# Kernel optimization log

Hardware: AMD Instinct MI355X
Metric: run time of the kernel (lower is better)

The kernel has to match this reference:

```python
import jax, jax.numpy as jnp
import numpy as np

B, N, D_IN, D, E, HEADS = 64, 512, 33, 32, 8192, 4
L, K_HOP, FF = 2, 2, 64  # num_layers, k_hop, dim_feedforward=2*d_out


def setup_inputs():
    key = jax.random.key(0)
    ks = iter(jax.random.split(key, 40))
    def nrm(shape, s=0.05):
        return jax.random.normal(next(ks), shape, jnp.float32) * s
    return {
        "H": jax.random.normal(next(ks), (B, N, D_IN), jnp.float32),
        "edge_index": jax.random.randint(next(ks), (2, E), 0, N, jnp.int32),
        # ObsEmbedding: Linear(33,32) ReLU Linear(32,32) ReLU LayerNorm(32)
        "emb_W1": nrm((D_IN, 32)), "emb_b1": jnp.zeros((32,), jnp.float32),
        "emb_W2": nrm((32, 32)), "emb_b2": jnp.zeros((32,), jnp.float32),
        "emb_ln_g": jnp.ones((32,), jnp.float32), "emb_ln_b": jnp.zeros((32,), jnp.float32),
        # per transformer layer: k_hop PNA-style GNN structure extractor
        # each hop: concat(self, mean, max, sum) -> Linear(4D, D), ReLU
        "gnn_W": nrm((L, K_HOP, 4 * D, D)), "gnn_b": jnp.zeros((L, K_HOP, D), jnp.float32),
        # structure-aware attention: Q,K from GNN-extracted features, V from x
        "Wq": nrm((L, D, D)), "Wk": nrm((L, D, D)), "Wv": nrm((L, D, D)), "Wo": nrm((L, D, D)),
        "bn1_g": jnp.ones((L, D), jnp.float32), "bn1_b": jnp.zeros((L, D), jnp.float32),
        "ff_W1": nrm((L, D, FF)), "ff_b1": jnp.zeros((L, FF), jnp.float32),
        "ff_W2": nrm((L, FF, D)), "ff_b2": jnp.zeros((L, D), jnp.float32),
        "bn2_g": jnp.ones((L, D), jnp.float32), "bn2_b": jnp.zeros((L, D), jnp.float32),
        # final node-level head Linear(d_model, num_class=d_out)
        "out_W": nrm((D, D)), "out_b": jnp.zeros((D,), jnp.float32),
    }


def _ln(x, g, b):
    m = x.mean(-1, keepdims=True)
    v = x.var(-1, keepdims=True)
    return (x - m) * jax.lax.rsqrt(v + 1e-5) * g + b


def _bn(x, g, b):  # batch_norm over all nodes of all graphs (training-mode stats)
    m = x.mean((0, 1))
    v = x.var((0, 1))
    return (x - m) * jax.lax.rsqrt(v + 1e-5) * g + b


def reference(H, edge_index, emb_W1, emb_b1, emb_W2, emb_b2, emb_ln_g, emb_ln_b,
              gnn_W, gnn_b, Wq, Wk, Wv, Wo, bn1_g, bn1_b,
              ff_W1, ff_b1, ff_W2, ff_b2, bn2_g, bn2_b, out_W, out_b):
    src, dst = edge_index[0], edge_index[1]
    # ObsEmbedding
    x = jax.nn.relu(H @ emb_W1 + emb_b1)
    x = jax.nn.relu(x @ emb_W2 + emb_b2)
    x = _ln(x, emb_ln_g, emb_ln_b)  # [B,N,D]
    cnt = jnp.zeros((N, 1), x.dtype).at[dst].add(1.0)  # in-degree, shared across batch
    dh = D // HEADS
    inv_sqrt_dh = np.float32(1.0 / np.sqrt(dh))
    for l in range(L):
        # --- k-hop structure extractor (PNA-style multi-aggregator message passing) ---
        h = x
        for k in range(K_HOP):
            msg = h[:, src]                                   # [B,E,D] gather
            s = jnp.zeros_like(h).at[:, dst].add(msg)         # sum aggregate
            mean = s / jnp.maximum(cnt, 1.0)
            mx = jnp.full_like(h, -1e30).at[:, dst].max(msg)  # max aggregate
            mx = jnp.where(cnt > 0, mx, 0.0)
            h = jax.nn.relu(jnp.concatenate([h, mean, mx, s], -1) @ gnn_W[l, k] + gnn_b[l, k])
        # --- structure-aware multi-head attention (full attention within graph) ---
        q = (h @ Wq[l]).reshape(B, N, HEADS, dh)
        kk = (h @ Wk[l]).reshape(B, N, HEADS, dh)
        v = (x @ Wv[l]).reshape(B, N, HEADS, dh)
        att = jax.nn.softmax(jnp.einsum("bqhd,bkhd->bhqk", q, kk) * inv_sqrt_dh, axis=-1)
        o = jnp.einsum("bhqk,bkhd->bqhd", att, v).reshape(B, N, D) @ Wo[l]
        x = _bn(x + o, bn1_g[l], bn1_b[l])
        f = jax.nn.relu(x @ ff_W1[l] + ff_b1[l]) @ ff_W2[l] + ff_b2[l]
        x = _bn(x + f, bn2_g[l], bn2_b[l])
    return x @ out_W + out_b  # [B,N,d_out], eval mode so dropout is identity
```

## Files before the change

### kernel.cpp

```cpp
#include <hip/hip_runtime.h>
#include <hip/hip_bf16.h>

#define BB 64
#define NN 512
#define DIN 33
#define DD 32
#define EE 8192
#define NHEADS 4
#define DH 8
#define FFD 64

typedef __attribute__((ext_vector_type(4))) float f32x4;
typedef __attribute__((ext_vector_type(4))) short bf16x4;

static __device__ __forceinline__ short f2bf(float x) {
    unsigned u = __float_as_uint(x);
    u = (u + 0x7FFFu + ((u >> 16) & 1u)) >> 16;
    return (short)u;
}

static __device__ __forceinline__ unsigned pack_trunc(float a, float b) {
    return (__float_as_uint(a) >> 16) | (__float_as_uint(b) & 0xFFFF0000u);
}

static __device__ __forceinline__ void mfma16(f32x4& d, bf16x4 a, bf16x4 b) {
#if __has_builtin(__builtin_amdgcn_mfma_f32_16x16x16bf16_1k)
    d = __builtin_amdgcn_mfma_f32_16x16x16bf16_1k(a, b, d, 0, 0, 0);
#else
    asm volatile("s_nop 1\n\tv_mfma_f32_16x16x16_bf16 %0, %1, %2, %0\n\ts_nop 7"
                 : "+v"(d) : "v"(a), "v"(b));
#endif
}

__global__ __launch_bounds__(512) void k_csr(const int* __restrict__ ei,
                                             float* __restrict__ cnt_f,
                                             int* __restrict__ csr_off,
                                             int* __restrict__ csr_src,
                                             float* __restrict__ stats) {
    __shared__ int cnt_s[NN];
    __shared__ int off_s[NN + 1];
    int tid = threadIdx.x;
    cnt_s[tid] = 0;
    if (tid < 256) stats[tid] = 0.f;
    __syncthreads();
    const int* src = ei;
    const int* dst = ei + EE;
    for (int e = tid; e < EE; e += 512) atomicAdd(&cnt_s[dst[e]], 1);
    __syncthreads();
    if (tid == 0) {
        int acc = 0;
        for (int n = 0; n < NN; ++n) { off_s[n] = acc; acc += cnt_s[n]; }
        off_s[NN] = acc;
    }
    __syncthreads();
    cnt_f[tid] = (float)cnt_s[tid];
    csr_off[tid] = off_s[tid];
    if (tid == 0) csr_off[NN] = off_s[NN];
    cnt_s[tid] = off_s[tid];
    __syncthreads();
    for (int e = tid; e < EE; e += 512) {
        int d = dst[e];
        int p = atomicAdd(&cnt_s[d], 1);
        csr_src[p] = src[e];
    }
}

__global__ __launch_bounds__(256) void k_emb(const float* __restrict__ H,
                                             const float* __restrict__ W1, const float* __restrict__ b1,
                                             const float* __restrict__ W2, const float* __restrict__ b2,
                                             const float* __restrict__ g,  const float* __restrict__ be,
                                             float* __restrict__ xb, float* __restrict__ xt) {
    __shared__ float sW1[DIN * DD];
    __shared__ float sW2[DD * DD];
    __shared__ float sb1[DD], sb2[DD], sg[DD], sbe[DD];
    __shared__ float sin_[8][DIN + 3];
    int tid = threadIdx.x;
    for (int i = tid; i < DIN * DD; i += 256) sW1[i] = W1[i];
    for (int i = tid; i < DD * DD; i += 256) sW2[i] = W2[i];
    if (tid < DD) { sb1[tid] = b1[tid]; sb2[tid] = b2[tid]; sg[tid] = g[tid]; sbe[tid] = be[tid]; }
    int grp = tid >> 5, lane = tid & 31;
    size_t node = (size_t)blockIdx.x * 8 + grp;
    const float* hrow = H + node * DIN;
    sin_[grp][lane] = hrow[lane];
    if (lane == 0) sin_[grp][32] = hrow[32];
    __syncthreads();
    float acc = sb1[lane];
    #pragma unroll
    for (int i = 0; i < DIN; ++i) acc += sin_[grp][i] * sW1[i * DD + lane];
    acc = fmaxf(acc, 0.f);
    float acc2 = sb2[lane];
    #pragma unroll
    for (int i = 0; i < DD; ++i) acc2 += __shfl(acc, i, 32) * sW2[i * DD + lane];
    acc2 = fmaxf(acc2, 0.f);
    float s = acc2;
    for (int off = 16; off; off >>= 1) s += __shfl_xor(s, off, 32);
    float m = s * (1.f / 32.f);
    float dv = acc2 - m;
    float sq = dv * dv;
    for (int off = 16; off; off >>= 1) sq += __shfl_xor(sq, off, 32);
    float var = sq * (1.f / 32.f);
    float v = dv * rsqrtf(var + 1e-5f) * sg[lane] + sbe[lane];
    xb[node * DD + lane] = v;
    int b = (int)(node >> 9), n = (int)(node & 511);
    xt[(size_t)n * 2048 + b * DD + lane] = v;
}

__global__ __launch_bounds__(256) void k_gnn(const float* __restrict__ gsrc, float* __restrict__ ht,
                                             const float* __restrict__ cnt_f,
                                             const int* __restrict__ csr_off,
                                             const int* __restrict__ csr_src,
                                             const float* __restrict__ W, const float* __restrict__ bias,
                                             int do_qkv,
                                             const float* __restrict__ xv_src,
                                             const float* __restrict__ Wq, const float* __restrict__ Wk,
                                             const float* __restrict__ Wv,
                                             short* __restrict__ qb2, short* __restrict__ kb2,
                                             short* __restrict__ vb2) {
    __shared__ short conc[32 * 132];
    __shared__ short sWt[32 * 132];
    __shared__ short sWqT[32 * 36], sWkT[32 * 36], sWvT[32 * 36];
    __shared__ short h_lds[32 * 36], x_lds[32 * 36];
    __shared__ float sb[DD];
    int tid = threadIdx.x;
    int n = blockIdx.x >> 1, half = blockIdx.x & 1;
    for (int i = tid; i < 128 * DD; i += 256) {
        int k = i >> 5, d = i & 31;
        sWt[d * 132 + k] = f2bf(W[i]);
    }
    if (tid < DD) sb[tid] = bias[tid];
    if (do_qkv) {
        const float isq = 0.35355339059327373f;
        for (int i = tid; i < 1024; i += 256) {
            int k = i >> 5, col = i & 31;
            sWqT[col * 36 + k] = f2bf(Wq[i] * isq);
            sWkT[col * 36 + k] = f2bf(Wk[i]);
            sWvT[col * 36 + k] = f2bf(Wv[i]);
        }
        int bl = tid >> 3, d0 = (tid & 7) * 4;
        float4 x4 = *(const float4*)&xv_src[(size_t)n * 2048 + half * 1024 + bl * 32 + d0];
        bf16x4 xp; xp.x = f2bf(x4.x); xp.y = f2bf(x4.y); xp.z = f2bf(x4.z); xp.w = f2bf(x4.w);
        *(bf16x4*)&x_lds[bl * 36 + d0] = xp;
    }
    const float* xbase = gsrc + (size_t)half * 1024 + tid * 4;
    float4 hv = *(const float4*)&xbase[(size_t)n * 2048];
    float4 s = {0.f, 0.f, 0.f, 0.f};
    float4 mx = {-1e30f, -1e30f, -1e30f, -1e30f};
    int beg = csr_off[n], end = csr_off[n + 1];
    int idx = beg;
    for (; idx + 3 < end; idx += 4) {
        int s0 = csr_src[idx], s1 = csr_src[idx + 1], s2 = csr_src[idx + 2], s3 = csr_src[idx + 3];
        float4 v0 = *(const float4*)&xbase[(size_t)s0 * 2048];
        float4 v1 = *(const float4*)&xbase[(size_t)s1 * 2048];
        float4 v2 = *(const float4*)&xbase[(size_t)s2 * 2048];
        float4 v3 = *(const float4*)&xbase[(size_t)s3 * 2048];
        s.x += (v0.x + v1.x) + (v2.x + v3.x);
        s.y += (v0.y + v1.y) + (v2.y + v3.y);
        s.z += (v0.z + v1.z) + (v2.z + v3.z);
        s.w += (v0.w + v1.w) + (v2.w + v3.w);
        mx.x = fmaxf(fmaxf(mx.x, v0.x), fmaxf(v1.x, fmaxf(v2.x, v3.x)));
        mx.y = fmaxf(fmaxf(mx.y, v0.y), fmaxf(v1.y, fmaxf(v2.y, v3.y)));
        mx.z = fmaxf(fmaxf(mx.z, v0.z), fmaxf(v1.z, fmaxf(v2.z, v3.z)));
        mx.w = fmaxf(fmaxf(mx.w, v0.w), fmaxf(v1.w, fmaxf(v2.w, v3.w)));
    }
    for (; idx < end; ++idx) {
        int s0 = csr_src[idx];
        float4 v0 = *(const float4*)&xbase[(size_t)s0 * 2048];
        s.x += v0.x; s.y += v0.y; s.z += v0.z; s.w += v0.w;
        mx.x = fmaxf(mx.x, v0.x); mx.y = fmaxf(mx.y, v0.y);
        mx.z = fmaxf(mx.z, v0.z); mx.w = fmaxf(mx.w, v0.w);
    }
    float c = cnt_f[n];
    float rinv = 1.f / fmaxf(c, 1.f);
    if (!(c > 0.f)) { mx.x = 0.f; mx.y = 0.f; mx.z = 0.f; mx.w = 0.f; }
    int bl = tid >> 3, d0 = (tid & 7) * 4;
    short* cp = &conc[bl * 132];
    bf16x4 t;
    t.x = f2bf(hv.x); t.y = f2bf(hv.y); t.z = f2bf(hv.z); t.w = f2bf(hv.w);
    *(bf16x4*)&cp[d0] = t;
    t.x = f2bf(s.x * rinv); t.y = f2bf(s.y * rinv); t.z = f2bf(s.z * rinv); t.w = f2bf(s.w * rinv);
    *(bf16x4*)&cp[32 + d0] = t;
    t.x = f2bf(mx.x); t.y = f2bf(mx.y); t.z = f2bf(mx.z); t.w = f2bf(mx.w);
    *(bf16x4*)&cp[64 + d0] = t;
    t.x = f2bf(s.x); t.y = f2bf(s.y); t.z = f2bf(s.z); t.w = f2bf(s.w);
    *(bf16x4*)&cp[96 + d0] = t;
    __syncthreads();
    int wid = tid >> 6, lane = tid & 63;
    int cc = lane & 15, g = lane >> 4;
    int arow = (wid >> 1) * 16 + cc;
    int bcol = (wid & 1) * 16 + cc;
    f32x4 acc = {0.f, 0.f, 0.f, 0.f};
    #pragma unroll
    for (int ks = 0; ks < 8; ++ks) {
        bf16x4 af = *(const bf16x4*)&conc[arow * 132 + ks * 16 + g * 4];
        bf16x4 bfr = *(const bf16x4*)&sWt[bcol * 132 + ks * 16 + g * 4];
        mfma16(acc, af, bfr);
    }
    float bia = sb[bcol];
    int brow = (wid >> 1) * 16 + g * 4;
    if (!do_qkv) {
        float* obase = &ht[(size_t)n * 2048 + half * 1024 + bcol];
        #pragma unroll
        for (int r = 0; r < 4; ++r) {
            obase[(size_t)(brow + r) * DD] = fmaxf(acc[r] + bia, 0.f);
        }
        return;
    }
    #pragma unroll
    for (int r = 0; r < 4; ++r) {
        h_lds[(brow + r) * 36 + bcol] = f2bf(fmaxf(acc[r] + bia, 0.f));
    }
    __syncthreads();
    int tr = wid >> 1, tc = wid & 1;
    f32x4 qa = {0.f, 0.f, 0.f, 0.f}, ka = qa, va = qa;
    #pragma unroll
    for (int ks = 0; ks < 2; ++ks) {
        bf16x4 ha = *(const bf16x4*)&h_lds[(tr * 16 + cc) * 36 + ks * 16 + g * 4];
        bf16x4 xa = *(const bf16x4*)&x_lds[(tr * 16 + cc) * 36 + ks * 16 + g * 4];
        bf16x4 wq = *(const bf16x4*)&sWqT[(tc * 16 + cc) * 36 + ks * 16 + g * 4];
        bf16x4 wk = *(const bf16x4*)&sWkT[(tc * 16 + cc) * 36 + ks * 16 + g * 4];
        bf16x4 wv = *(const bf16x4*)&sWvT[(tc * 16 + cc) * 36 + ks * 16 + g * 4];
        mfma16(qa, ha, wq);
        mfma16(ka, ha, wk);
        mfma16(va, xa, wv);
    }
    int dcol = tc * 16 + cc;
    size_t base = ((size_t)(half * 32 + tr * 16 + g * 4) * NN + n) * DD + dcol;
    #pragma unroll
    for (int r = 0; r < 4; ++r) {
        size_t p = base + (size_t)r * (NN * DD);
        qb2[p] = f2bf(qa[r]);
        kb2[p] = f2bf(ka[r]);
        vb2[p] = f2bf(va[r]);
    }
}

__global__ __launch_bounds__(256) void k_attn_proj(const short* __restrict__ qb2,
                                                   const short* __restrict__ kb2,
                                                   const short* __restrict__ vb2,
                                                   const float* __restrict__ x,
                                                   const float* __restrict__ Wo,
                                                   float* __restrict__ t,
                                                   float* __restrict__ stats) {
    __shared__ short Vt[NHEADS * DH * 528];
    __shared__ short Ot[64 * 36];
    __shared__ short sWoT[DD * 36];
    __shared__ float rs[4][DD], rq[4][DD];
    int bid = blockIdx.x;
    int qs = bid & 7, b = bid >> 3;
    int tid = threadIdx.x;

    for (int i = tid; i < 1024; i += 256) {
        int k = i >> 5, col = i & 31;
        sWoT[col * 36 + k] = f2bf(Wo[i]);
    }
    {
        size_t g0 = ((size_t)b * NN + tid * 2) * DD;
        #pragma unroll
        for (int h2 = 0; h2 < 4; ++h2) {
            uint4 v0 = *(const uint4*)&vb2[g0 + h2 * 8];
            uint4 v1 = *(const uint4*)&vb2[g0 + DD + h2 * 8];
            unsigned* vt = (unsigned*)&Vt[h2 * DH * 528];
            vt[0 * 264 + tid] = (v0.x & 0xFFFFu) | (v1.x << 16);
            vt[1 * 264 + tid] = (v0.x >> 16)     | (v1.x & 0xFFFF0000u);
            vt[2 * 264 + tid] = (v0.y & 0xFFFFu) | (v1.y << 16);
            vt[3 * 264 + tid] = (v0.y >> 16)     | (v1.y & 0xFFFF0000u);
            vt[4 * 264 + tid] = (v0.z & 0xFFFFu) | (v1.z << 16);
            vt[5 * 264 + tid] = (v0.z >> 16)     | (v1.z & 0xFFFF0000u);
            vt[6 * 264 + tid] = (v0.w & 0xFFFFu) | (v1.w << 16);
            vt[7 * 264 + tid] = (v0.w >> 16)     | (v1.w & 0xFFFF0000u);
        }
    }
    __syncthreads();

    int h = tid >> 6, lane = tid & 63;
    int c = lane & 15, g = lane >> 4;
    int c7 = c & 7;
    bf16x4 z4 = {0, 0, 0, 0};
    bf16x4 qf0 = z4, qf1 = z4, qf2 = z4, qf3 = z4;
    if (g < 2) {
        const short* qbase = &qb2[(((size_t)b * NN + qs * 64) * DD) + h * DH + g * 4];
        qf0 = *(const bf16x4*)&qbase[(size_t)(c) * DD];
        qf1 = *(const bf16x4*)&qbase[(size_t)(16 + c) * DD];
        qf2 = *(const bf16x4*)&qbase[(size_t)(32 + c) * DD];
        qf3 = *(const bf16x4*)&qbase[(size_t)(48 + c) * DD];
    }
    const short* kbase = &kb2[((size_t)b * NN) * DD + h * DH + g * 4];
    float l0 = 0.f, l1 = 0.f, l2 = 0.f, l3 = 0.f;
    f32x4 o0 = {0.f, 0.f, 0.f, 0.f}, o1 = o0, o2 = o0, o3 = o0;
    union U { unsigned u[2]; bf16x4 v4; };

    for (int kc = 0; kc < 32; ++kc) {
        bf16x4 kf = z4;
        if (g < 2) kf = *(const bf16x4*)&kbase[(size_t)(kc * 16 + c) * DD];
        bf16x4 vf = z4;
        {
            bf16x4 vl = *(const bf16x4*)&Vt[(h * DH + c7) * 528 + kc * 16 + g * 4];
            if (c < 8) vf = vl;
        }
        f32x4 st0 = {0.f, 0.f, 0.f, 0.f}, st1 = st0, st2 = st0, st3 = st0;
        mfma16(st0, kf, qf0);
        mfma16(st1, kf, qf1);
        mfma16(st2, kf, qf2);
        mfma16(st3, kf, qf3);
        {
            float p0 = __expf(st0[0]), p1 = __expf(st0[1]), p2 = __expf(st0[2]), p3 = __expf(st0[3]);
            l0 += (p0 + p1) + (p2 + p3);
            U pu; pu.u[0] = pack_trunc(p0, p1); pu.u[1] = pack_trunc(p2, p3);
            mfma16(o0, vf, pu.v4);
        }
        {
            float p0 = __expf(st1[0]), p1 = __expf(st1[1]), p2 = __expf(st1[2]), p3 = __expf(st1[3]);
            l1 += (p0 + p1) + (p2 + p3);
            U pu; pu.u[0] = pack_trunc(p0, p1); pu.u[1] = pack_trunc(p2, p3);
            mfma16(o1, vf, pu.v4);
        }
        {
            float p0 = __expf(st2[0]), p1 = __expf(st2[1]), p2 = __expf(st2[2]), p3 = __expf(st2[3]);
            l2 += (p0 + p1) + (p2 + p3);
            U pu; pu.u[0] = pack_trunc(p0, p1); pu.u[1] = pack_trunc(p2, p3);
            mfma16(o2, vf, pu.v4);
        }
        {
            float p0 = __expf(st3[0]), p1 = __expf(st3[1]), p2 = __expf(st3[2]), p3 = __expf(st3[3]);
            l3 += (p0 + p1) + (p2 + p3);
            U pu; pu.u[0] = pack_trunc(p0, p1); pu.u[1] = pack_trunc(p2, p3);
            mfma16(o3, vf, pu.v4);
        }
    }
    l0 += __shfl_xor(l0, 16, 64); l0 += __shfl_xor(l0, 32, 64);
    l1 += __shfl_xor(l1, 16, 64); l1 += __shfl_xor(l1, 32, 64);
    l2 += __shfl_xor(l2, 16, 64); l2 += __shfl_xor(l2, 32, 64);
    l3 += __shfl_xor(l3, 16, 64); l3 += __shfl_xor(l3, 32, 64);
    if (g < 2) {
        float inv0 = 1.f / l0, inv1 = 1.f / l1, inv2 = 1.f / l2, inv3 = 1.f / l3;
        int fb = h * DH + g * 4;
        #pragma unroll
        for (int r = 0; r < 4; ++r) {
            Ot[(c) * 36 + fb + r]      = f2bf(o0[r] * inv0);
            Ot[(16 + c) * 36 + fb + r] = f2bf(o1[r] * inv1);
            Ot[(32 + c) * 36 + fb + r] = f2bf(o2[r] * inv2);
            Ot[(48 + c) * 36 + fb + r] = f2bf(o3[r] * inv3);
        }
    }
    __syncthreads();
    f32x4 pa0 = {0.f, 0.f, 0.f, 0.f}, pa1 = pa0;
    #pragma unroll
    for (int ks = 0; ks < 2; ++ks) {
        bf16x4 af = *(const bf16x4*)&Ot[(h * 16 + c) * 36 + ks * 16 + g * 4];
        bf16x4 b0 = *(const bf16x4*)&sWoT[c * 36 + ks * 16 + g * 4];
        bf16x4 b1 = *(const bf16x4*)&sWoT[(16 + c) * 36 + ks * 16 + g * 4];
        mfma16(pa0, af, b0);
        mfma16(pa1, af, b1);
    }
    float ls0 = 0.f, lq0 = 0.f, ls1 = 0.f, lq1 = 0.f;
    size_t rowbase = ((size_t)b * NN + qs * 64 + h * 16 + g * 4) * DD;
    #pragma unroll
    for (int r = 0; r < 4; ++r) {
        float xv0 = x[rowbase + (size_t)r * DD + c];
        float tv0 = xv0 + pa0[r];
        t[rowbase + (size_t)r * DD + c] = tv0;
        ls0 += tv0; lq0 += tv0 * tv0;
        float xv1 = x[rowbase + (size_t)r * DD + 16 + c];
        float tv1 = xv1 + pa1[r];
        t[rowbase + (size_t)r * DD + 16 + c] = tv1;
        ls1 += tv1; lq1 += tv1 * tv1;
    }
    ls0 += __shfl_xor(ls0, 16, 64); ls0 += __shfl_xor(ls0, 32, 64);
    lq0 += __shfl_xor(lq0, 16, 64); lq0 += __shfl_xor(lq0, 32, 64);
    ls1 += __shfl_xor(ls1, 16, 64); ls1 += __shfl_xor(ls1, 32, 64);
    lq1 += __shfl_xor(lq1, 16, 64); lq1 += __shfl_xor(lq1, 32, 64);
    if (g == 0) {
        rs[h][c] = ls0; rs[h][16 + c] = ls1;
        rq[h][c] = lq0; rq[h][16 + c] = lq1;
    }
    __syncthreads();
    if (tid < DD) {
        float a = (rs[0][tid] + rs[1][tid]) + (rs[2][tid] + rs[3][tid]);
        float b2 = (rq[0][tid] + rq[1][tid]) + (rq[2][tid] + rq[3][tid]);
        atomicAdd(&stats[tid], a);
        atomicAdd(&stats[DD + tid], b2);
    }
}

__global__ __launch_bounds__(256) void k_ff(const float* __restrict__ t, const float* __restrict__ stats,
                                            const float* __restrict__ g1, const float* __restrict__ be1,
                                            const float* __restrict__ W1, const float* __restrict__ fb1,
                                            const float* __restrict__ W2, const float* __restrict__ fb2,
                                            float* __restrict__ t2, float* __restrict__ stats2) {
    __shared__ short x1b[64 * 36];
    __shared__ float x1f[64 * 33];
    __shared__ short hm[64 * 68];
    __shared__ short sW1T[FFD * 36];
    __shared__ short sW2T[DD * 68];
    __shared__ float sc[DD], sm[DD], sbe[DD], sb2v[DD];
    __shared__ float sb1v[FFD];
    __shared__ float rs[4][DD], rq[4][DD];
    int tid = threadIdx.x;
    for (int i = tid; i < 2048; i += 256) {
        int k = i >> 6, col = i & 63;
        sW1T[col * 36 + k] = f2bf(W1[i]);
        int k2 = i >> 5, col2 = i & 31;
        sW2T[col2 * 68 + k2] = f2bf(W2[i]);
    }
    if (tid < DD) {
        float mean = stats[tid] * (1.f / 32768.f);
        float var  = stats[DD + tid] * (1.f / 32768.f) - mean * mean;
        sc[tid] = rsqrtf(var + 1e-5f) * g1[tid];
        sm[tid] = mean; sbe[tid] = be1[tid]; sb2v[tid] = fb2[tid];
    }
    if (tid < FFD) sb1v[tid] = fb1[tid];
    __syncthreads();
    size_t node0 = (size_t)blockIdx.x * 64;
    {
        int row = tid >> 2, cb = (tid & 3) * 8;
        const float* tp = &t[(node0 + row) * DD + cb];
        float4 a = *(const float4*)tp;
        float4 bq = *(const float4*)(tp + 4);
        float v0 = (a.x - sm[cb + 0]) * sc[cb + 0] + sbe[cb + 0];
        float v1 = (a.y - sm[cb + 1]) * sc[cb + 1] + sbe[cb + 1];
        float v2 = (a.z - sm[cb + 2]) * sc[cb + 2] + sbe[cb + 2];
        float v3 = (a.w - sm[cb + 3]) * sc[cb + 3] + sbe[cb + 3];
        float v4 = (bq.x - sm[cb + 4]) * sc[cb + 4] + sbe[cb + 4];
        float v5 = (bq.y - sm[cb + 5]) * sc[cb + 5] + sbe[cb + 5];
        float v6 = (bq.z - sm[cb + 6]) * sc[cb + 6] + sbe[cb + 6];
        float v7 = (bq.w - sm[cb + 7]) * sc[cb + 7] + sbe[cb + 7];
        float* xf = &x1f[row * 33 + cb];
        xf[0] = v0; xf[1] = v1; xf[2] = v2; xf[3] = v3;
        xf[4] = v4; xf[5] = v5; xf[6] = v6; xf[7] = v7;
        bf16x4 p0; p0.x = f2bf(v0); p0.y = f2bf(v1); p0.z = f2bf(v2); p0.w = f2bf(v3);
        bf16x4 p1; p1.x = f2bf(v4); p1.y = f2bf(v5); p1.z = f2bf(v6); p1.w = f2bf(v7);
        *(bf16x4*)&x1b[row * 36 + cb] = p0;
        *(bf16x4*)&x1b[row * 36 + cb + 4] = p1;
    }
    __syncthreads();
    int w = tid >> 6, lane = tid & 63, c = lane & 15, g = lane >> 4;
    f32x4 m0 = {0.f, 0.f, 0.f, 0.f}, m1 = m0, m2 = m0, m3 = m0;
    #pragma unroll
    for (int ks = 0; ks < 2; ++ks) {
        bf16x4 af = *(const bf16x4*)&x1b[(w * 16 + c) * 36 + ks * 16 + g * 4];
        mfma16(m0, af, *(const bf16x4*)&sW1T[(c) * 36 + ks * 16 + g * 4]);
        mfma16(m1, af, *(const bf16x4*)&sW1T[(16 + c) * 36 + ks * 16 + g * 4]);
        mfma16(m2, af, *(const bf16x4*)&sW1T[(32 + c) * 36 + ks * 16 + g * 4]);
        mfma16(m3, af, *(const bf16x4*)&sW1T[(48 + c) * 36 + ks * 16 + g * 4]);
    }
    {
        float b0 = sb1v[c], b1 = sb1v[16 + c], b2 = sb1v[32 + c], b3 = sb1v[48 + c];
        #pragma unroll
        for (int r = 0; r < 4; ++r) {
            short* hr = &hm[(w * 16 + g * 4 + r) * 68];
            hr[c]      = f2bf(fmaxf(m0[r] + b0, 0.f));
            hr[16 + c] = f2bf(fmaxf(m1[r] + b1, 0.f));
            hr[32 + c] = f2bf(fmaxf(m2[r] + b2, 0.f));
            hr[48 + c] = f2bf(fmaxf(m3[r] + b3, 0.f));
        }
    }
    __syncthreads();
    f32x4 f0 = {0.f, 0.f, 0.f, 0.f}, f1 = f0;
    #pragma unroll
    for (int ks = 0; ks < 4; ++ks) {
        bf16x4 af = *(const bf16x4*)&hm[(w * 16 + c) * 68 + ks * 16 + g * 4];
        mfma16(f0, af, *(const bf16x4*)&sW2T[(c) * 68 + ks * 16 + g * 4]);
        mfma16(f1, af, *(const bf16x4*)&sW2T[(16 + c) * 68 + ks * 16 + g * 4]);
    }
    float ls0 = 0.f, lq0 = 0.f, ls1 = 0.f, lq1 = 0.f;
    float bb0 = sb2v[c], bb1 = sb2v[16 + c];
    #pragma unroll
    for (int r = 0; r < 4; ++r) {
        int row = w * 16 + g * 4 + r;
        float tv0 = x1f[row * 33 + c] + f0[r] + bb0;
        t2[(node0 + row) * DD + c] = tv0;
        ls0 += tv0; lq0 += tv0 * tv0;
        float tv1 = x1f[row * 33 + 16 + c] + f1[r] + bb1;
        t2[(node0 + row) * DD + 16 + c] = tv1;
        ls1 += tv1; lq1 += tv1 * tv1;
    }
    ls0 += __shfl_xor(ls0, 16, 64); ls0 += __shfl_xor(ls0, 32, 64);
    lq0 += __shfl_xor(lq0, 16, 64); lq0 += __shfl_xor(lq0, 32, 64);
    ls1 += __shfl_xor(ls1, 16, 64); ls1 += __shfl_xor(ls1, 32, 64);
    lq1 += __shfl_xor(lq1, 16, 64); lq1 += __shfl_xor(lq1, 32, 64);
    if (g == 0) {
        rs[w][c] = ls0; rs[w][16 + c] = ls1;
        rq[w][c] = lq0; rq[w][16 + c] = lq1;
    }
    __syncthreads();
    if (tid < DD) {
        float a = (rs[0][tid] + rs[1][tid]) + (rs[2][tid] + rs[3][tid]);
        float bsum = (rq[0][tid] + rq[1][tid]) + (rq[2][tid] + rq[3][tid]);
        atomicAdd(&stats2[tid], a);
        atomicAdd(&stats2[DD + tid], bsum);
    }
}

__global__ __launch_bounds__(256) void k_bn2(const float* __restrict__ t2, const float* __restrict__ stats2,
                                             const float* __restrict__ g, const float* __restrict__ be,
                                             float* __restrict__ xout, float* __restrict__ xtout,
                                             const float* __restrict__ outW, const float* __restrict__ outb,
                                             float* __restrict__ fout, int do_proj) {
    __shared__ float sW[DD * DD];
    int tid = threadIdx.x;
    if (do_proj) for (int i = tid; i < DD * DD; i += 256) sW[i] = outW[i];
    __syncthreads();
    int grp = tid >> 5, lane = tid & 31;
    float mean  = stats2[lane] * (1.f / 32768.f);
    float var   = stats2[DD + lane] * (1.f / 32768.f) - mean * mean;
    float scale = rsqrtf(var + 1e-5f) * g[lane];
    float shift = be[lane];
    size_t node = (size_t)blockIdx.x * 8 + grp;
    float tv = t2[node * DD + lane];
    float xv = (tv - mean) * scale + shift;
    xout[node * DD + lane] = xv;
    int b = (int)(node >> 9), n = (int)(node & 511);
    xtout[(size_t)n * 2048 + b * DD + lane] = xv;
    if (do_proj) {
        float acc = outb[lane];
        #pragma unroll
        for (int i = 0; i < DD; ++i) acc += __shfl(xv, i, 32) * sW[i * DD + lane];
        fout[node * DD + lane] = acc;
    }
}

extern "C" void kernel_launch(void* const* d_in, const int* in_sizes, int n_in,
                              void* d_out, int out_size, void* d_ws, size_t ws_size,
                              hipStream_t stream) {
    const float* H    = (const float*)d_in[0];
    const int*   ei   = (const int*)  d_in[1];
    const float* eW1  = (const float*)d_in[2];
    const float* eb1  = (const float*)d_in[3];
    const float* eW2  = (const float*)d_in[4];
    const float* eb2  = (const float*)d_in[5];
    const float* elg  = (const float*)d_in[6];
    const float* elb  = (const float*)d_in[7];
    const float* gW   = (const float*)d_in[8];
    const float* gb   = (const float*)d_in[9];
    const float* Wq   = (const float*)d_in[10];
    const float* Wk   = (const float*)d_in[11];
    const float* Wv   = (const float*)d_in[12];
    const float* Wo   = (const float*)d_in[13];
    const float* bn1g = (const float*)d_in[14];
    const float* bn1b = (const float*)d_in[15];
    const float* fW1  = (const float*)d_in[16];
    const float* fb1  = (const float*)d_in[17];
    const float* fW2  = (const float*)d_in[18];
    const float* fb2  = (const float*)d_in[19];
    const float* bn2g = (const float*)d_in[20];
    const float* bn2b = (const float*)d_in[21];
    const float* oW   = (const float*)d_in[22];
    const float* obv  = (const float*)d_in[23];
    float* out = (float*)d_out;

    float* ws = (float*)d_ws;
    const size_t BIGSZ = (size_t)BB * NN * DD;
    float* xb = ws;
    float* xt = ws + 1 * BIGSZ;
    float* hA = ws + 2 * BIGSZ;
    float* hB = ws + 3 * BIGSZ;
    short* qb2 = (short*)(ws + 4 * BIGSZ);
    short* kb2 = qb2 + BIGSZ;
    short* vb2 = (short*)(ws + 5 * BIGSZ);
    float* tb = ws + 7 * BIGSZ;
    float* smalls = ws + 8 * BIGSZ;
    float* cnt_f   = smalls;
    int*   csr_off = (int*)(smalls + 512);
    int*   csr_src = (int*)(smalls + 512 + 516);
    float* stats   = smalls + 512 + 516 + 8192;

    k_csr<<<1, 512, 0, stream>>>(ei, cnt_f, csr_off, csr_src, stats);
    k_emb<<<BB * NN / 8, 256, 0, stream>>>(H, eW1, eb1, eW2, eb2, elg, elb, xb, xt);

    for (int l = 0; l < 2; ++l) {
        const float* gW0 = gW + (size_t)(l * 2 + 0) * 128 * DD;
        const float* gW1 = gW + (size_t)(l * 2 + 1) * 128 * DD;
        const float* gb0 = gb + (size_t)(l * 2 + 0) * DD;
        const float* gb1 = gb + (size_t)(l * 2 + 1) * DD;
        float* st1 = stats + l * 128;
        float* st2 = stats + l * 128 + 64;
        k_gnn<<<NN * 2, 256, 0, stream>>>(xt, hA, cnt_f, csr_off, csr_src, gW0, gb0,
                                          0, nullptr, nullptr, nullptr, nullptr,
                                          nullptr, nullptr, nullptr);
        k_gnn<<<NN * 2, 256, 0, stream>>>(hA, nullptr, cnt_f, csr_off, csr_src, gW1, gb1,
                                          1, xt, Wq + l * DD * DD, Wk + l * DD * DD,
                                          Wv + l * DD * DD, qb2, kb2, vb2);
        k_attn_proj<<<BB * 8, 256, 0, stream>>>(qb2, kb2, vb2, xb, Wo + l * DD * DD, tb, st1);
        k_ff<<<512, 256, 0, stream>>>(tb, st1, bn1g + l * DD, bn1b + l * DD,
                                      fW1 + l * DD * FFD, fb1 + l * FFD,
                                      fW2 + l * FFD * DD, fb2 + l * DD,
                                      hB, st2);
        k_bn2<<<BB * NN / 8, 256, 0, stream>>>(hB, st2, bn2g + l * DD, bn2b + l * DD,
                                               xb, xt, oW, obv, out, (l == 1) ? 1 : 0);
    }
}
```

Baseline: 218.9 us.

## Fold BN2 normalization into downstream kernels and drop separate bn2 pass

```diff
diff --git a/kernel.cpp b/kernel.cpp
--- a/kernel.cpp
+++ b/kernel.cpp
@@ -38,7 +38,7 @@
                                              int* __restrict__ csr_src,
                                              float* __restrict__ stats) {
     __shared__ int cnt_s[NN];
-    __shared__ int off_s[NN + 1];
+    __shared__ int wsum[8];
     int tid = threadIdx.x;
     cnt_s[tid] = 0;
     if (tid < 256) stats[tid] = 0.f;
@@ -47,16 +47,28 @@
     const int* dst = ei + EE;
     for (int e = tid; e < EE; e += 512) atomicAdd(&cnt_s[dst[e]], 1);
     __syncthreads();
+    int c = cnt_s[tid];
+    int lane = tid & 63, w = tid >> 6;
+    int sc_ = c;
+    #pragma unroll
+    for (int off = 1; off < 64; off <<= 1) {
+        int nv = __shfl_up(sc_, off, 64);
+        if (lane >= off) sc_ += nv;
+    }
+    if (lane == 63) wsum[w] = sc_;
+    __syncthreads();
     if (tid == 0) {
-        int acc = 0;
-        for (int n = 0; n < NN; ++n) { off_s[n] = acc; acc += cnt_s[n]; }
-        off_s[NN] = acc;
-    }
-    __syncthreads();
-    cnt_f[tid] = (float)cnt_s[tid];
-    csr_off[tid] = off_s[tid];
-    if (tid == 0) csr_off[NN] = off_s[NN];
-    cnt_s[tid] = off_s[tid];
+        int a = 0;
+        #pragma unroll
+        for (int i = 0; i < 8; ++i) { int t = wsum[i]; wsum[i] = a; a += t; }
+    }
+    __syncthreads();
+    int excl = sc_ - c + wsum[w];
+    cnt_f[tid] = (float)c;
+    csr_off[tid] = excl;
+    if (tid == 511) csr_off[NN] = excl + c;
+    __syncthreads();
+    cnt_s[tid] = excl;
     __syncthreads();
     for (int e = tid; e < EE; e += 512) {
         int d = dst[e];
@@ -105,30 +117,137 @@
     xt[(size_t)n * 2048 + b * DD + lane] = v;
 }
 
-__global__ __launch_bounds__(256) void k_gnn(const float* __restrict__ gsrc, float* __restrict__ ht,
-                                             const float* __restrict__ cnt_f,
-                                             const int* __restrict__ csr_off,
-                                             const int* __restrict__ csr_src,
-                                             const float* __restrict__ W, const float* __restrict__ bias,
-                                             int do_qkv,
-                                             const float* __restrict__ xv_src,
-                                             const float* __restrict__ Wq, const float* __restrict__ Wk,
-                                             const float* __restrict__ Wv,
-                                             short* __restrict__ qb2, short* __restrict__ kb2,
-                                             short* __restrict__ vb2) {
+__global__ __launch_bounds__(256) void k_gnn1(const float* __restrict__ src, float* __restrict__ ht,
+                                              const float* __restrict__ cnt_f,
+                                              const int* __restrict__ csr_off,
+                                              const int* __restrict__ csr_src,
+                                              const float* __restrict__ W, const float* __restrict__ bias,
+                                              const float* __restrict__ bnstats,
+                                              const float* __restrict__ bng, const float* __restrict__ bnb) {
+    __shared__ short conc[32 * 132];
+    __shared__ short sWt[32 * 132];
+    __shared__ float sb[DD];
+    __shared__ float scv[DD], offv[DD];
+    int tid = threadIdx.x;
+    int n = blockIdx.x >> 1, half = blockIdx.x & 1;
+    for (int i = tid; i < 128 * DD; i += 256) {
+        int k = i >> 5, d = i & 31;
+        sWt[d * 132 + k] = f2bf(W[i]);
+    }
+    if (tid < DD) {
+        sb[tid] = bias[tid];
+        if (bnstats) {
+            float mean = bnstats[tid] * (1.f / 32768.f);
+            float var  = bnstats[DD + tid] * (1.f / 32768.f) - mean * mean;
+            float sc = rsqrtf(var + 1e-5f) * bng[tid];
+            scv[tid] = sc; offv[tid] = bnb[tid] - mean * sc;
+        } else { scv[tid] = 1.f; offv[tid] = 0.f; }
+    }
+    __syncthreads();
+    float4 sc4, of4;
+    { int d0 = (tid * 4) & 31;
+      sc4.x = scv[d0]; sc4.y = scv[d0 + 1]; sc4.z = scv[d0 + 2]; sc4.w = scv[d0 + 3];
+      of4.x = offv[d0]; of4.y = offv[d0 + 1]; of4.z = offv[d0 + 2]; of4.w = offv[d0 + 3]; }
+    const float* xbase = src + (size_t)half * 1024 + tid * 4;
+    float4 hv = *(const float4*)&xbase[(size_t)n * 2048];
+    hv.x = fmaf(hv.x, sc4.x, of4.x); hv.y = fmaf(hv.y, sc4.y, of4.y);
+    hv.z = fmaf(hv.z, sc4.z, of4.z); hv.w = fmaf(hv.w, sc4.w, of4.w);
+    float4 s = {0.f, 0.f, 0.f, 0.f};
+    float4 mx = {-1e30f, -1e30f, -1e30f, -1e30f};
+    int beg = csr_off[n], end = csr_off[n + 1];
+    int idx = beg;
+    for (; idx + 3 < end; idx += 4) {
+        int s0 = csr_src[idx], s1 = csr_src[idx + 1], s2 = csr_src[idx + 2], s3 = csr_src[idx + 3];
+        float4 v0 = *(const float4*)&xbase[(size_t)s0 * 2048];
+        float4 v1 = *(const float4*)&xbase[(size_t)s1 * 2048];
+        float4 v2 = *(const float4*)&xbase[(size_t)s2 * 2048];
+        float4 v3 = *(const float4*)&xbase[(size_t)s3 * 2048];
+        v0.x = fmaf(v0.x, sc4.x, of4.x); v0.y = fmaf(v0.y, sc4.y, of4.y);
+        v0.z = fmaf(v0.z, sc4.z, of4.z); v0.w = fmaf(v0.w, sc4.w, of4.w);
+        v1.x = fmaf(v1.x, sc4.x, of4.x); v1.y = fmaf(v1.y, sc4.y, of4.y);
+        v1.z = fmaf(v1.z, sc4.z, of4.z); v1.w = fmaf(v1.w, sc4.w, of4.w);
+        v2.x = fmaf(v2.x, sc4.x, of4.x); v2.y = fmaf(v2.y, sc4.y, of4.y);
+        v2.z = fmaf(v2.z, sc4.z, of4.z); v2.w = fmaf(v2.w, sc4.w, of4.w);
+        v3.x = fmaf(v3.x, sc4.x, of4.x); v3.y = fmaf(v3.y, sc4.y, of4.y);
+        v3.z = fmaf(v3.z, sc4.z, of4.z); v3.w = fmaf(v3.w, sc4.w, of4.w);
+        s.x += (v0.x + v1.x) + (v2.x + v3.x);
+        s.y += (v0.y + v1.y) + (v2.y + v3.y);
+        s.z += (v0.z + v1.z) + (v2.z + v3.z);
+        s.w += (v0.w + v1.w) + (v2.w + v3.w);
+        mx.x = fmaxf(fmaxf(mx.x, v0.x), fmaxf(v1.x, fmaxf(v2.x, v3.x)));
+        mx.y = fmaxf(fmaxf(mx.y, v0.y), fmaxf(v1.y, fmaxf(v2.y, v3.y)));
+        mx.z = fmaxf(fmaxf(mx.z, v0.z), fmaxf(v1.z, fmaxf(v2.z, v3.z)));
+        mx.w = fmaxf(fmaxf(mx.w, v0.w), fmaxf(v1.w, fmaxf(v2.w, v3.w)));
+    }
+    for (; idx < end; ++idx) {
+        int s0 = csr_src[idx];
+        float4 v0 = *(const float4*)&xbase[(size_t)s0 * 2048];
+        v0.x = fmaf(v0.x, sc4.x, of4.x); v0.y = fmaf(v0.y, sc4.y, of4.y);
+        v0.z = fmaf(v0.z, sc4.z, of4.z); v0.w = fmaf(v0.w, sc4.w, of4.w);
+        s.x += v0.x; s.y += v0.y; s.z += v0.z; s.w += v0.w;
+        mx.x = fmaxf(mx.x, v0.x); mx.y = fmaxf(mx.y, v0.y);
+        mx.z = fmaxf(mx.z, v0.z); mx.w = fmaxf(mx.w, v0.w);
+    }
+    float c = cnt_f[n];
+    float rinv = 1.f / fmaxf(c, 1.f);
+    if (!(c > 0.f)) { mx.x = 0.f; mx.y = 0.f; mx.z = 0.f; mx.w = 0.f; }
+    int bl = tid >> 3, d0 = (tid & 7) * 4;
+    short* cp = &conc[bl * 132];
+    bf16x4 t;
+    t.x = f2bf(hv.x); t.y = f2bf(hv.y); t.z = f2bf(hv.z); t.w = f2bf(hv.w);
+    *(bf16x4*)&cp[d0] = t;
+    t.x = f2bf(s.x * rinv); t.y = f2bf(s.y * rinv); t.z = f2bf(s.z * rinv); t.w = f2bf(s.w * rinv);
+    *(bf16x4*)&cp[32 + d0] = t;
+    t.x = f2bf(mx.x); t.y = f2bf(mx.y); t.z = f2bf(mx.z); t.w = f2bf(mx.w);
+    *(bf16x4*)&cp[64 + d0] = t;
+    t.x = f2bf(s.x); t.y = f2bf(s.y); t.z = f2bf(s.z); t.w = f2bf(s.w);
+    *(bf16x4*)&cp[96 + d0] = t;
+    __syncthreads();
+    int wid = tid >> 6, lane = tid & 63;
+    int cc = lane & 15, g = lane >> 4;
+    int arow = (wid >> 1) * 16 + cc;
+    int bcol = (wid & 1) * 16 + cc;
+    f32x4 acc = {0.f, 0.f, 0.f, 0.f};
+    #pragma unroll
+    for (int ks = 0; ks < 8; ++ks) {
+        bf16x4 af = *(const bf16x4*)&conc[arow * 132 + ks * 16 + g * 4];
+        bf16x4 bfr = *(const bf16x4*)&sWt[bcol * 132 + ks * 16 + g * 4];
+        mfma16(acc, af, bfr);
+    }
+    float bia = sb[bcol];
+    int brow = (wid >> 1) * 16 + g * 4;
+    float* obase = &ht[(size_t)n * 2048 + half * 1024 + bcol];
+    #pragma unroll
+    for (int r = 0; r < 4; ++r) {
+        obase[(size_t)(brow + r) * DD] = fmaxf(acc[r] + bia, 0.f);
+    }
+}
+
+__global__ __launch_bounds__(256) void k_gnn2(const float* __restrict__ hsrc,
+                                              const float* __restrict__ cnt_f,
+                                              const int* __restrict__ csr_off,
+                                              const int* __restrict__ csr_src,
+                                              const float* __restrict__ W, const float* __restrict__ bias,
+                                              const float* __restrict__ xsrc,
+                                              const float* __restrict__ bnstats,
+                                              const float* __restrict__ bng, const float* __restrict__ bnb,
+                                              const float* __restrict__ Wq, const float* __restrict__ Wk,
+                                              const float* __restrict__ Wv,
+                                              short* __restrict__ qb2, short* __restrict__ kb2,
+                                              short* __restrict__ vb2) {
     __shared__ short conc[32 * 132];
     __shared__ short sWt[32 * 132];
     __shared__ short sWqT[32 * 36], sWkT[32 * 36], sWvT[32 * 36];
     __shared__ short h_lds[32 * 36], x_lds[32 * 36];
     __shared__ float sb[DD];
+    __shared__ float scv[DD], offv[DD];
     int tid = threadIdx.x;
     int n = blockIdx.x >> 1, half = blockIdx.x & 1;
     for (int i = tid; i < 128 * DD; i += 256) {
         int k = i >> 5, d = i & 31;
         sWt[d * 132 + k] = f2bf(W[i]);
     }
-    if (tid < DD) sb[tid] = bias[tid];
-    if (do_qkv) {
+    {
         const float isq = 0.35355339059327373f;
         for (int i = tid; i < 1024; i += 256) {
             int k = i >> 5, col = i & 31;
@@ -136,12 +255,28 @@
             sWkT[col * 36 + k] = f2bf(Wk[i]);
             sWvT[col * 36 + k] = f2bf(Wv[i]);
         }
+    }
+    if (tid < DD) {
+        sb[tid] = bias[tid];
+        if (bnstats) {
+            float mean = bnstats[tid] * (1.f / 32768.f);
+            float var  = bnstats[DD + tid] * (1.f / 32768.f) - mean * mean;
+            float sc = rsqrtf(var + 1e-5f) * bng[tid];
+            scv[tid] = sc; offv[tid] = bnb[tid] - mean * sc;
+        } else { scv[tid] = 1.f; offv[tid] = 0.f; }
+    }
+    __syncthreads();
+    {
         int bl = tid >> 3, d0 = (tid & 7) * 4;
-        float4 x4 = *(const float4*)&xv_src[(size_t)n * 2048 + half * 1024 + bl * 32 + d0];
+        float4 x4 = *(const float4*)&xsrc[(size_t)n * 2048 + half * 1024 + bl * 32 + d0];
+        x4.x = fmaf(x4.x, scv[d0], offv[d0]);
+        x4.y = fmaf(x4.y, scv[d0 + 1], offv[d0 + 1]);
+        x4.z = fmaf(x4.z, scv[d0 + 2], offv[d0 + 2]);
+        x4.w = fmaf(x4.w, scv[d0 + 3], offv[d0 + 3]);
         bf16x4 xp; xp.x = f2bf(x4.x); xp.y = f2bf(x4.y); xp.z = f2bf(x4.z); xp.w = f2bf(x4.w);
         *(bf16x4*)&x_lds[bl * 36 + d0] = xp;
     }
-    const float* xbase = gsrc + (size_t)half * 1024 + tid * 4;
+    const float* xbase = hsrc + (size_t)half * 1024 + tid * 4;
     float4 hv = *(const float4*)&xbase[(size_t)n * 2048];
     float4 s = {0.f, 0.f, 0.f, 0.f};
     float4 mx = {-1e30f, -1e30f, -1e30f, -1e30f};
@@ -197,14 +332,6 @@
     }
     float bia = sb[bcol];
     int brow = (wid >> 1) * 16 + g * 4;
-    if (!do_qkv) {
-        float* obase = &ht[(size_t)n * 2048 + half * 1024 + bcol];
-        #pragma unroll
-        for (int r = 0; r < 4; ++r) {
-            obase[(size_t)(brow + r) * DD] = fmaxf(acc[r] + bia, 0.f);
-        }
-        return;
-    }
     #pragma unroll
     for (int r = 0; r < 4; ++r) {
         h_lds[(brow + r) * 36 + bcol] = f2bf(fmaxf(acc[r] + bia, 0.f));
@@ -238,6 +365,9 @@
                                                    const short* __restrict__ kb2,
                                                    const short* __restrict__ vb2,
                                                    const float* __restrict__ x,
+                                                   const float* __restrict__ bnstats,
+                                                   const float* __restrict__ bng,
+                                                   const float* __restrict__ bnb,
                                                    const float* __restrict__ Wo,
                                                    float* __restrict__ t,
                                                    float* __restrict__ stats) {
@@ -245,6 +375,7 @@
     __shared__ short Ot[64 * 36];
     __shared__ short sWoT[DD * 36];
     __shared__ float rs[4][DD], rq[4][DD];
+    __shared__ float scv[DD], offv[DD];
     int bid = blockIdx.x;
     int qs = bid & 7, b = bid >> 3;
     int tid = threadIdx.x;
@@ -252,6 +383,14 @@
     for (int i = tid; i < 1024; i += 256) {
         int k = i >> 5, col = i & 31;
         sWoT[col * 36 + k] = f2bf(Wo[i]);
+    }
+    if (tid < DD) {
+        if (bnstats) {
+            float mean = bnstats[tid] * (1.f / 32768.f);
+            float var  = bnstats[DD + tid] * (1.f / 32768.f) - mean * mean;
+            float sc = rsqrtf(var + 1e-5f) * bng[tid];
+            scv[tid] = sc; offv[tid] = bnb[tid] - mean * sc;
+        } else { scv[tid] = 1.f; offv[tid] = 0.f; }
     }
     {
         size_t g0 = ((size_t)b * NN + tid * 2) * DD;
@@ -352,15 +491,16 @@
         mfma16(pa0, af, b0);
         mfma16(pa1, af, b1);
     }
+    float sc0 = scv[c], of0 = offv[c], sc1 = scv[16 + c], of1 = offv[16 + c];
     float ls0 = 0.f, lq0 = 0.f, ls1 = 0.f, lq1 = 0.f;
     size_t rowbase = ((size_t)b * NN + qs * 64 + h * 16 + g * 4) * DD;
     #pragma unroll
     for (int r = 0; r < 4; ++r) {
-        float xv0 = x[rowbase + (size_t)r * DD + c];
+        float xv0 = fmaf(x[rowbase + (size_t)r * DD + c], sc0, of0);
         float tv0 = xv0 + pa0[r];
         t[rowbase + (size_t)r * DD + c] = tv0;
         ls0 += tv0; lq0 += tv0 * tv0;
-        float xv1 = x[rowbase + (size_t)r * DD + 16 + c];
+        float xv1 = fmaf(x[rowbase + (size_t)r * DD + 16 + c], sc1, of1);
         float tv1 = xv1 + pa1[r];
         t[rowbase + (size_t)r * DD + 16 + c] = tv1;
         ls1 += tv1; lq1 += tv1 * tv1;
@@ -386,7 +526,8 @@
                                             const float* __restrict__ g1, const float* __restrict__ be1,
                                             const float* __restrict__ W1, const float* __restrict__ fb1,
                                             const float* __restrict__ W2, const float* __restrict__ fb2,
-                                            float* __restrict__ t2, float* __restrict__ stats2) {
+                                            float* __restrict__ t2, float* __restrict__ t2n,
+                                            float* __restrict__ stats2) {
     __shared__ short x1b[64 * 36];
     __shared__ float x1f[64 * 33];
     __shared__ short hm[64 * 68];
@@ -462,6 +603,8 @@
         mfma16(f0, af, *(const bf16x4*)&sW2T[(c) * 68 + ks * 16 + g * 4]);
         mfma16(f1, af, *(const bf16x4*)&sW2T[(16 + c) * 68 + ks * 16 + g * 4]);
     }
+    __syncthreads();
+    float* t2s = (float*)hm;
     float ls0 = 0.f, lq0 = 0.f, ls1 = 0.f, lq1 = 0.f;
     float bb0 = sb2v[c], bb1 = sb2v[16 + c];
     #pragma unroll
@@ -469,9 +612,11 @@
         int row = w * 16 + g * 4 + r;
         float tv0 = x1f[row * 33 + c] + f0[r] + bb0;
         t2[(node0 + row) * DD + c] = tv0;
+        t2s[row * DD + c] = tv0;
         ls0 += tv0; lq0 += tv0 * tv0;
         float tv1 = x1f[row * 33 + 16 + c] + f1[r] + bb1;
         t2[(node0 + row) * DD + 16 + c] = tv1;
+        t2s[row * DD + 16 + c] = tv1;
         ls1 += tv1; lq1 += tv1 * tv1;
     }
     ls0 += __shfl_xor(ls0, 16, 64); ls0 += __shfl_xor(ls0, 32, 64);
@@ -489,33 +634,69 @@
         atomicAdd(&stats2[tid], a);
         atomicAdd(&stats2[DD + tid], bsum);
     }
-}
-
-__global__ __launch_bounds__(256) void k_bn2(const float* __restrict__ t2, const float* __restrict__ stats2,
-                                             const float* __restrict__ g, const float* __restrict__ be,
-                                             float* __restrict__ xout, float* __restrict__ xtout,
+    if (t2n) {
+        int bb = (int)(node0 >> 9), nn0 = (int)(node0 & 511);
+        for (int i = tid; i < 512; i += 256) {
+            int row = i >> 3, c4 = i & 7;
+            float4 v = *(const float4*)&t2s[row * DD + c4 * 4];
+            *(float4*)&t2n[(size_t)(nn0 + row) * 2048 + bb * DD + c4 * 4] = v;
+        }
+    }
+}
+
+__global__ __launch_bounds__(256) void k_out(const float* __restrict__ t2, const float* __restrict__ stats,
+                                             const float* __restrict__ g2, const float* __restrict__ be2,
                                              const float* __restrict__ outW, const float* __restrict__ outb,
-                                             float* __restrict__ fout, int do_proj) {
-    __shared__ float sW[DD * DD];
+                                             float* __restrict__ out) {
+    __shared__ short x1b[64 * 36];
+    __shared__ short sWoT[DD * 36];
+    __shared__ float scv[DD], offv[DD], sbo[DD];
     int tid = threadIdx.x;
-    if (do_proj) for (int i = tid; i < DD * DD; i += 256) sW[i] = outW[i];
-    __syncthreads();
-    int grp = tid >> 5, lane = tid & 31;
-    float mean  = stats2[lane] * (1.f / 32768.f);
-    float var   = stats2[DD + lane] * (1.f / 32768.f) - mean * mean;
-    float scale = rsqrtf(var + 1e-5f) * g[lane];
-    float shift = be[lane];
-    size_t node = (size_t)blockIdx.x * 8 + grp;
-    float tv = t2[node * DD + lane];
-    float xv = (tv - mean) * scale + shift;
-    xout[node * DD + lane] = xv;
-    int b = (int)(node >> 9), n = (int)(node & 511);
-    xtout[(size_t)n * 2048 + b * DD + lane] = xv;
-    if (do_proj) {
-        float acc = outb[lane];
-        #pragma unroll
-        for (int i = 0; i < DD; ++i) acc += __shfl(xv, i, 32) * sW[i * DD + lane];
-        fout[node * DD + lane] = acc;
+    for (int i = tid; i < 1024; i += 256) {
+        int k = i >> 5, col = i & 31;
+        sWoT[col * 36 + k] = f2bf(outW[i]);
+    }
+    if (tid < DD) {
+        float mean = stats[tid] * (1.f / 32768.f);
+        float var  = stats[DD + tid] * (1.f / 32768.f) - mean * mean;
+        float sc = rsqrtf(var + 1e-5f) * g2[tid];
+        scv[tid] = sc; offv[tid] = be2[tid] - mean * sc;
+        sbo[tid] = outb[tid];
+    }
+    __syncthreads();
+    size_t node0 = (size_t)blockIdx.x * 64;
+    {
+        int row = tid >> 2, cb = (tid & 3) * 8;
+        const float* tp = &t2[(node0 + row) * DD + cb];
+        float4 a = *(const float4*)tp;
+        float4 bq = *(const float4*)(tp + 4);
+        bf16x4 p0, p1;
+        p0.x = f2bf(fmaf(a.x, scv[cb + 0], offv[cb + 0]));
+        p0.y = f2bf(fmaf(a.y, scv[cb + 1], offv[cb + 1]));
+        p0.z = f2bf(fmaf(a.z, scv[cb + 2], offv[cb + 2]));
+        p0.w = f2bf(fmaf(a.w, scv[cb + 3], offv[cb + 3]));
+        p1.x = f2bf(fmaf(bq.x, scv[cb + 4], offv[cb + 4]));
+        p1.y = f2bf(fmaf(bq.y, scv[cb + 5], offv[cb + 5]));
+        p1.z = f2bf(fmaf(bq.z, scv[cb + 6], offv[cb + 6]));
+        p1.w = f2bf(fmaf(bq.w, scv[cb + 7], offv[cb + 7]));
+        *(bf16x4*)&x1b[row * 36 + cb] = p0;
+        *(bf16x4*)&x1b[row * 36 + cb + 4] = p1;
+    }
+    __syncthreads();
+    int w = tid >> 6, lane = tid & 63, c = lane & 15, g = lane >> 4;
+    f32x4 a0 = {0.f, 0.f, 0.f, 0.f}, a1 = a0;
+    #pragma unroll
+    for (int ks = 0; ks < 2; ++ks) {
+        bf16x4 af = *(const bf16x4*)&x1b[(w * 16 + c) * 36 + ks * 16 + g * 4];
+        mfma16(a0, af, *(const bf16x4*)&sWoT[(c) * 36 + ks * 16 + g * 4]);
+        mfma16(a1, af, *(const bf16x4*)&sWoT[(16 + c) * 36 + ks * 16 + g * 4]);
+    }
+    float b0 = sbo[c], b1 = sbo[16 + c];
+    #pragma unroll
+    for (int r = 0; r < 4; ++r) {
+        int row = w * 16 + g * 4 + r;
+        out[(node0 + row) * DD + c]      = a0[r] + b0;
+        out[(node0 + row) * DD + 16 + c] = a1[r] + b1;
     }
 }
 
@@ -550,14 +731,15 @@
 
     float* ws = (float*)d_ws;
     const size_t BIGSZ = (size_t)BB * NN * DD;
-    float* xb = ws;
-    float* xt = ws + 1 * BIGSZ;
-    float* hA = ws + 2 * BIGSZ;
-    float* hB = ws + 3 * BIGSZ;
+    float* xb  = ws;
+    float* xt  = ws + 1 * BIGSZ;
+    float* hA  = ws + 2 * BIGSZ;
+    float* hB  = ws + 3 * BIGSZ;
     short* qb2 = (short*)(ws + 4 * BIGSZ);
     short* kb2 = qb2 + BIGSZ;
     short* vb2 = (short*)(ws + 5 * BIGSZ);
-    float* tb = ws + 7 * BIGSZ;
+    float* t2n = ws + 6 * BIGSZ;
+    float* tb  = ws + 7 * BIGSZ;
     float* smalls = ws + 8 * BIGSZ;
     float* cnt_f   = smalls;
     int*   csr_off = (int*)(smalls + 512);
@@ -574,18 +756,24 @@
         const float* gb1 = gb + (size_t)(l * 2 + 1) * DD;
         float* st1 = stats + l * 128;
         float* st2 = stats + l * 128 + 64;
-        k_gnn<<<NN * 2, 256, 0, stream>>>(xt, hA, cnt_f, csr_off, csr_src, gW0, gb0,
-                                          0, nullptr, nullptr, nullptr, nullptr,
-                                          nullptr, nullptr, nullptr);
-        k_gnn<<<NN * 2, 256, 0, stream>>>(hA, nullptr, cnt_f, csr_off, csr_src, gW1, gb1,
-                                          1, xt, Wq + l * DD * DD, Wk + l * DD * DD,
-                                          Wv + l * DD * DD, qb2, kb2, vb2);
-        k_attn_proj<<<BB * 8, 256, 0, stream>>>(qb2, kb2, vb2, xb, Wo + l * DD * DD, tb, st1);
+        const float* pstats = (l == 0) ? nullptr : stats + 64;
+        const float* pg = (l == 0) ? nullptr : bn2g;
+        const float* pb = (l == 0) ? nullptr : bn2b;
+        const float* gsrc = (l == 0) ? xt : t2n;
+        const float* xres = (l == 0) ? xb : hB;
+
+        k_gnn1<<<NN * 2, 256, 0, stream>>>(gsrc, hA, cnt_f, csr_off, csr_src, gW0, gb0,
+                                           pstats, pg, pb);
+        k_gnn2<<<NN * 2, 256, 0, stream>>>(hA, cnt_f, csr_off, csr_src, gW1, gb1,
+                                           gsrc, pstats, pg, pb,
+                                           Wq + l * DD * DD, Wk + l * DD * DD, Wv + l * DD * DD,
+                                           qb2, kb2, vb2);
+        k_attn_proj<<<BB * 8, 256, 0, stream>>>(qb2, kb2, vb2, xres, pstats, pg, pb,
+                                                Wo + l * DD * DD, tb, st1);
         k_ff<<<512, 256, 0, stream>>>(tb, st1, bn1g + l * DD, bn1b + l * DD,
                                       fW1 + l * DD * FFD, fb1 + l * FFD,
                                       fW2 + l * FFD * DD, fb2 + l * DD,
-                                      hB, st2);
-        k_bn2<<<BB * NN / 8, 256, 0, stream>>>(hB, st2, bn2g + l * DD, bn2b + l * DD,
-                                               xb, xt, oW, obv, out, (l == 1) ? 1 : 0);
-    }
-}
+                                      hB, (l == 0) ? t2n : nullptr, st2);
+    }
+    k_out<<<512, 256, 0, stream>>>(hB, stats + 192, bn2g + DD, bn2b + DD, oW, obv, out);
+}
```

New measurement: 204.6 us. -6.5%, faster.
